# Kernel tuning notes

Measured on AMD Instinct MI355X. Metric: run time of the kernel, lower is better.

Reference implementation:

```python
import jax, jax.numpy as jnp
import numpy as np
from jax import lax

V, D, H, HR = 32000, 512, 1024, 2
T_SRC, T_TGT, T_REF, B, NREF = 128, 128, 32, 64, 4


def _gru_scan(x_emb, lengths, h0, Wih, Whh, bih, bhh):
    """Masked GRU over padded [T,B,D]; equivalent to torch pack->GRU->unpack.
    Returns (outputs [T,B,h] zeroed past lengths, final hidden [B,h])."""
    T = x_emb.shape[0]
    xW = jnp.einsum('tbd,gd->tbg', x_emb, Wih) + bih  # [T,B,3h] input-gate preacts

    def step(h, inp):
        xw, t = inp
        hw = h @ Whh.T + bhh
        xr, xz, xn = jnp.split(xw, 3, axis=-1)
        hr, hz, hn = jnp.split(hw, 3, axis=-1)
        r = jax.nn.sigmoid(xr + hr)
        z = jax.nn.sigmoid(xz + hz)
        n = jnp.tanh(xn + r * hn)
        h_new = (1.0 - z) * n + z * h
        m = (t < lengths)[:, None]
        h_next = jnp.where(m, h_new, h)   # freeze hidden past length (packing)
        out = jnp.where(m, h_new, 0.0)    # unpack pads with zeros
        return h_next, out

    hT, outs = lax.scan(step, h0, (xW, jnp.arange(T)))
    return outs, hT


def setup_inputs() -> dict:
    key = jax.random.key(0)
    ks = jax.random.split(key, 32)

    def u(k, shape, fan):
        lim = 1.0 / np.sqrt(fan)
        return jax.random.uniform(k, shape, jnp.float32, -lim, lim)

    inp = {}
    inp['tgt'] = jax.random.randint(ks[0], (T_TGT, B), 0, V)
    inp['tgt_lengths'] = jax.random.randint(ks[1], (B,), 1, T_TGT + 1)
    inp['src'] = jax.random.randint(ks[2], (T_SRC, B), 0, V)
    inp['src_lengths'] = jax.random.randint(ks[3], (B,), 1, T_SRC + 1)
    inp['ref_ids'] = jax.random.randint(ks[4], (NREF, T_REF, B), 0, V)
    inp['ref_lengths'] = jax.random.randint(ks[5], (NREF, B), 1, T_REF + 1)
    inp['emb'] = jax.random.normal(ks[6], (V, D), jnp.float32) * 0.02
    inp['src_Wih'] = u(ks[7], (3 * H, D), H)
    inp['src_Whh'] = u(ks[8], (3 * H, H), H)
    inp['src_bih'] = u(ks[9], (3 * H,), H)
    inp['src_bhh'] = u(ks[10], (3 * H,), H)
    inp['tgt_Wih'] = u(ks[11], (3 * H, D), H)
    inp['tgt_Whh'] = u(ks[12], (3 * H, H), H)
    inp['tgt_bih'] = u(ks[13], (3 * H,), H)
    inp['tgt_bhh'] = u(ks[14], (3 * H,), H)
    inp['ref_Wih'] = u(ks[15], (3 * HR, D), HR)
    inp['ref_Whh'] = u(ks[16], (3 * HR, HR), HR)
    inp['ref_bih'] = u(ks[17], (3 * HR,), HR)
    inp['ref_bhh'] = u(ks[18], (3 * HR,), HR)
    inp['p1_W'] = u(ks[19], (64, H), H)
    inp['p1_b'] = u(ks[20], (64,), H)
    inp['p2_W'] = u(ks[21], (2, 64), 64)
    inp['p2_b'] = u(ks[22], (2,), 64)
    return inp


def reference(tgt, tgt_lengths, src, src_lengths, ref_ids, ref_lengths, emb,
              src_Wih, src_Whh, src_bih, src_bhh,
              tgt_Wih, tgt_Whh, tgt_bih, tgt_bhh,
              ref_Wih, ref_Whh, ref_bih, ref_bhh,
              p1_W, p1_b, p2_W, p2_b):
    # --- src encoder ---
    src_emb = emb[src]  # [T_SRC,B,D]
    h0 = jnp.zeros((src.shape[1], src_Whh.shape[1]), emb.dtype)
    _, src_hT = _gru_scan(src_emb, src_lengths, h0, src_Wih, src_Whh, src_bih, src_bhh)

    # --- ref encoders: original loops in Python over the ref list with
    # per-ref sort/pack/tiny-GRU; here vectorized with vmap over NREF.
    # (Output is computed, as torch eager does, but does not feed logits.)
    ref_emb = emb[ref_ids]  # [NREF,T_REF,B,D]
    h0r = jnp.zeros((ref_ids.shape[2], ref_Whh.shape[1]), emb.dtype)
    ref_context, ref_hidden = jax.vmap(
        lambda e, l: _gru_scan(e, l, h0r, ref_Wih, ref_Whh, ref_bih, ref_bhh)
    )(ref_emb, ref_lengths)
    del ref_context, ref_hidden

    # --- tgt decoder initialized from src final hidden ---
    tgt_emb = emb[tgt]
    _, tgt_hT = _gru_scan(tgt_emb, tgt_lengths, src_hT, tgt_Wih, tgt_Whh, tgt_bih, tgt_bhh)

    # --- projection head (dropout = identity in eval) ---
    logits = jnp.tanh(tgt_hT @ p1_W.T + p1_b) @ p2_W.T + p2_b  # [B,2]
    return logits
```

## Files before the change

kernel.cpp:

```cpp
#include <hip/hip_runtime.h>
#include <stdint.h>

typedef short short8 __attribute__((ext_vector_type(8)));
typedef float f32x4 __attribute__((ext_vector_type(4)));
typedef float f32x2 __attribute__((ext_vector_type(2)));
typedef unsigned long long u64;

#define TSEQ   128
#define BATCH  64
#define DIM    512
#define HID    1024
#define G3     3072
#define MROWS  (TSEQ * BATCH)
#define NB     32
#define HB     32

__device__ __forceinline__ unsigned short f2bf(float f) {
  union { float f; unsigned u; } v; v.f = f;
  unsigned u = v.u;
  return (unsigned short)((u + 0x7FFFu + ((u >> 16) & 1u)) >> 16);
}

__device__ __forceinline__ short8 pack8(f32x4 a, f32x4 b) {
  short8 r;
  r[0] = (short)f2bf(a.x); r[1] = (short)f2bf(a.y);
  r[2] = (short)f2bf(a.z); r[3] = (short)f2bf(a.w);
  r[4] = (short)f2bf(b.x); r[5] = (short)f2bf(b.y);
  r[6] = (short)f2bf(b.z); r[7] = (short)f2bf(b.w);
  return r;
}

__device__ __forceinline__ u64 packbf4(float a, float b, float c, float d) {
  return (u64)f2bf(a) | ((u64)f2bf(b) << 16) | ((u64)f2bf(c) << 32) | ((u64)f2bf(d) << 48);
}

__device__ __forceinline__ float sigm(float x) { return 1.0f / (1.0f + __expf(-x)); }
__device__ __forceinline__ float tanh_fast(float x) { return 2.0f / (1.0f + __expf(-2.0f * x)) - 1.0f; }

__global__ __launch_bounds__(256) void prep_kernel(
    const int* __restrict__ ids, const float* __restrict__ emb,
    const float* __restrict__ wih, unsigned short* __restrict__ X,
    unsigned short* __restrict__ Wb, unsigned int* bars, int nbar)
{
  int row = blockIdx.x;
  int tid = threadIdx.x;
  const float* srcp;
  unsigned short* dst;
  if (row < MROWS) {
    srcp = emb + (long)ids[row] * DIM;
    dst  = X + (long)row * DIM;
  } else {
    int wr = row - MROWS;
    srcp = wih + (long)wr * DIM;
    dst  = Wb + (long)wr * DIM;
  }
  int d = tid * 2;
  f32x2 v = *(const f32x2*)(srcp + d);
  unsigned pk = (unsigned)f2bf(v.x) | ((unsigned)f2bf(v.y) << 16);
  *(unsigned*)(dst + d) = pk;
  if (bars != nullptr && row == 0 && tid < nbar) bars[tid] = 0u;
}

#define BM 128
#define BN 128
#define BK 32

__global__ __launch_bounds__(256) void xw_gemm(
    const unsigned short* __restrict__ X,
    const unsigned short* __restrict__ W,
    const float* __restrict__ bih,
    float* __restrict__ out)
{
  __shared__ unsigned short As[BM * BK];
  __shared__ unsigned short Bs[BN * BK];
  int tid = threadIdx.x;
  int w = tid >> 6, l = tid & 63;
  int m0 = blockIdx.y * BM;
  int n0 = blockIdx.x * BN;
  int wr = w >> 1, wc = w & 1;

  int sr = tid >> 2, skq = tid & 3;
  int sr2 = sr + 64;
  int sgk  = (skq - (sr  >> 1)) & 3;
  int sgk2 = (skq - (sr2 >> 1)) & 3;
  const unsigned short* gA0 = X + (long)(m0 + sr ) * DIM + sgk  * 8;
  const unsigned short* gA1 = X + (long)(m0 + sr2) * DIM + sgk2 * 8;
  const unsigned short* gB0 = W + (long)(n0 + sr ) * DIM + sgk  * 8;
  const unsigned short* gB1 = W + (long)(n0 + sr2) * DIM + sgk2 * 8;
  unsigned short* lA0 = As + sr  * BK + skq * 8;
  unsigned short* lA1 = As + sr2 * BK + skq * 8;
  unsigned short* lB0 = Bs + sr  * BK + skq * 8;
  unsigned short* lB1 = Bs + sr2 * BK + skq * 8;

  f32x4 acc[4][4];
  #pragma unroll
  for (int mt = 0; mt < 4; ++mt)
    #pragma unroll
    for (int nt = 0; nt < 4; ++nt) acc[mt][nt] = (f32x4){};

  short8 va0 = *(const short8*)(gA0);
  short8 va1 = *(const short8*)(gA1);
  short8 vb0 = *(const short8*)(gB0);
  short8 vb1 = *(const short8*)(gB1);

  int fr = l & 15, fk = l >> 4;
  for (int kt = 0; kt < DIM / BK; ++kt) {
    __syncthreads();
    *(short8*)lA0 = va0; *(short8*)lA1 = va1;
    *(short8*)lB0 = vb0; *(short8*)lB1 = vb1;
    __syncthreads();
    if (kt + 1 < DIM / BK) {
      int ko = (kt + 1) * BK;
      va0 = *(const short8*)(gA0 + ko);
      va1 = *(const short8*)(gA1 + ko);
      vb0 = *(const short8*)(gB0 + ko);
      vb1 = *(const short8*)(gB1 + ko);
    }
    short8 af[4], bf[4];
    #pragma unroll
    for (int mt = 0; mt < 4; ++mt) {
      int r = wr * 64 + mt * 16 + fr;
      int slot = ((r >> 1) + fk) & 3;
      af[mt] = *(const short8*)(As + r * BK + slot * 8);
    }
    #pragma unroll
    for (int nt = 0; nt < 4; ++nt) {
      int r = wc * 64 + nt * 16 + fr;
      int slot = ((r >> 1) + fk) & 3;
      bf[nt] = *(const short8*)(Bs + r * BK + slot * 8);
    }
    #pragma unroll
    for (int mt = 0; mt < 4; ++mt)
      #pragma unroll
      for (int nt = 0; nt < 4; ++nt)
        acc[mt][nt] = __builtin_amdgcn_mfma_f32_16x16x32_bf16(af[mt], bf[nt], acc[mt][nt], 0, 0, 0);
  }

  #pragma unroll
  for (int nt = 0; nt < 4; ++nt) {
    int n = n0 + wc * 64 + nt * 16 + fr;
    float bias = bih[n];
    #pragma unroll
    for (int mt = 0; mt < 4; ++mt) {
      int mbase = m0 + wr * 64 + mt * 16 + fk * 4;
      #pragma unroll
      for (int r = 0; r < 4; ++r)
        out[(long)(mbase + r) * G3 + n] = acc[mt][nt][r] + bias;
    }
  }
}

#define MF(a, b, c) __builtin_amdgcn_mfma_f32_16x16x32_bf16(a, b, c, 0, 0, 0)

#define ISSUE(ss, kk) do { \
  asm volatile("global_load_dwordx4 %0, %1, off offset:%2 sc0 sc1" \
               : "=v"(bv[ss][0]) : "v"(ad0), "i"((kk) * 64) : "memory"); \
  asm volatile("global_load_dwordx4 %0, %1, off offset:%2 sc0 sc1" \
               : "=v"(bv[ss][1]) : "v"(ad1), "i"((kk) * 64) : "memory"); \
  asm volatile("global_load_dwordx4 %0, %1, off offset:%2 sc0 sc1" \
               : "=v"(bv[ss][2]) : "v"(ad2), "i"((kk) * 64) : "memory"); \
  asm volatile("global_load_dwordx4 %0, %1, off offset:%2 sc0 sc1" \
               : "=v"(bv[ss][3]) : "v"(ad3), "i"((kk) * 64) : "memory"); \
} while (0)

#define MF6(kk, ss, nt) \
  acc[0][nt] = MF(areg[0][kk], bv[ss][nt], acc[0][nt]); \
  acc[1][nt] = MF(areg[1][kk], bv[ss][nt], acc[1][nt]); \
  acc[2][nt] = MF(areg[2][kk], bv[ss][nt], acc[2][nt]); \
  acc[3][nt] = MF(areg[3][kk], bv[ss][nt], acc[3][nt]); \
  acc[4][nt] = MF(areg[4][kk], bv[ss][nt], acc[4][nt]); \
  acc[5][nt] = MF(areg[5][kk], bv[ss][nt], acc[5][nt]);

#define CONS(kk, ss, wn) do { \
  asm volatile("s_waitcnt vmcnt(" #wn ")" ::: "memory"); \
  __builtin_amdgcn_sched_barrier(0); \
  MF6(kk, ss, 0) MF6(kk, ss, 1) MF6(kk, ss, 2) MF6(kk, ss, 3) \
} while (0)

#define CONSI(kk, ss, wn, nk) do { CONS(kk, ss, wn); ISSUE(ss, nk); } while (0)

__global__ __launch_bounds__(256, 1) void gru_kernel(
    const float* __restrict__ Whh, const float* __restrict__ bhh,
    const float* __restrict__ xw, const int* __restrict__ lengths,
    u64* __restrict__ hbf,
    float* __restrict__ hf32,
    unsigned int* __restrict__ bar, int T, int initzero)
{
  const int tid = threadIdx.x;
  const int w = tid >> 6, l = tid & 63;
  const int fr = l & 15, fk = l >> 4;
  const int U0 = blockIdx.x * HB;

  short8 areg[6][8];
  #pragma unroll
  for (int mt = 0; mt < 6; ++mt) {
    const int m = mt * 16 + fr;
    const int gate = m >> 5, u = m & 31;
    const float* wp = Whh + (size_t)(gate * HID + U0 + u) * HID + w * 256 + fk * 8;
    #pragma unroll
    for (int ksl = 0; ksl < 8; ++ksl) {
      f32x4 a0 = *(const f32x4*)(wp + ksl * 32);
      f32x4 a1 = *(const f32x4*)(wp + ksl * 32 + 4);
      areg[mt][ksl] = pack8(a0, a1);
    }
  }

  const int gb = l;
  const int j0 = w * 8;
  const size_t hoff = (size_t)gb * (HID / 4) + (size_t)(U0 + j0) / 4;
  const int len_b = lengths[gb];

  float h[8];
  #pragma unroll
  for (int j = 0; j < 8; ++j)
    h[j] = initzero ? 0.0f : hf32[(size_t)gb * HID + U0 + j0 + j];

  __shared__ float red[2][96][67];
  __shared__ float bb[3][32];
  if (tid < 96) bb[tid >> 5][tid & 31] = bhh[(tid >> 5) * HID + U0 + (tid & 31)];

  f32x4 xrv[2], xzv[2], xnv[2];
  #define LOAD_XW(tt) do { \
    const float* xp_ = xw + ((size_t)(tt) * BATCH + gb) * G3 + U0 + j0; \
    xrv[0] = *(const f32x4*)(xp_);            xrv[1] = *(const f32x4*)(xp_ + 4); \
    xzv[0] = *(const f32x4*)(xp_ + HID);      xzv[1] = *(const f32x4*)(xp_ + HID + 4); \
    xnv[0] = *(const f32x4*)(xp_ + 2 * HID);  xnv[1] = *(const f32x4*)(xp_ + 2 * HID + 4); \
  } while (0)

  {
    union { u64 q[2]; f32x4 v4; } pk;
    pk.q[0] = packbf4(h[0], h[1], h[2], h[3]);
    pk.q[1] = packbf4(h[4], h[5], h[6], h[7]);
    uint64_t hw = (uint64_t)(hbf + hoff);
    asm volatile("global_store_dwordx4 %0, %1, off sc0 sc1" :: "v"(hw), "v"(pk.v4) : "memory");
    asm volatile("s_waitcnt vmcnt(0)" ::: "memory");
    __syncthreads();
    if (tid == 0)
      __hip_atomic_fetch_add(bar, 1u, __ATOMIC_RELAXED, __HIP_MEMORY_SCOPE_AGENT);
    LOAD_XW(0);
    if (tid == 0) {
      while (__hip_atomic_load(bar, __ATOMIC_RELAXED, __HIP_MEMORY_SCOPE_AGENT) < (unsigned)NB)
        __builtin_amdgcn_s_sleep(1);
    }
    __syncthreads();
  }

  for (int t = 0; t < T; ++t) {
    asm volatile("s_waitcnt vmcnt(0)" ::: "memory");

    const char* hbase = (const char*)hbf + (size_t)(t & 1) * (BATCH * (HID / 4) * 8);
    uint64_t ad0 = (uint64_t)(hbase + (size_t)(fr) * 2048 + w * 512 + fk * 16);
    uint64_t ad1 = ad0 + 16 * 2048;
    uint64_t ad2 = ad0 + 32 * 2048;
    uint64_t ad3 = ad0 + 48 * 2048;

    f32x4 acc[6][4];
    #pragma unroll
    for (int mt = 0; mt < 6; ++mt)
      #pragma unroll
      for (int nt = 0; nt < 4; ++nt) acc[mt][nt] = (f32x4){};

    short8 bv[6][4];
    ISSUE(0, 0); ISSUE(1, 1); ISSUE(2, 2); ISSUE(3, 3); ISSUE(4, 4); ISSUE(5, 5);
    CONSI(0, 0, 20, 6);
    CONSI(1, 1, 20, 7);
    CONS(2, 2, 20);
    CONS(3, 3, 16);
    CONS(4, 4, 12);
    CONS(5, 5, 8);
    CONS(6, 0, 4);
    CONS(7, 1, 0);

    if (w < 2) {
      #pragma unroll
      for (int mt = 0; mt < 6; ++mt)
        #pragma unroll
        for (int nt = 0; nt < 4; ++nt)
          #pragma unroll
          for (int r = 0; r < 4; ++r)
            red[w][mt * 16 + fk * 4 + r][nt * 16 + fr] = acc[mt][nt][r];
    }
    __syncthreads();
    if (w >= 2) {
      #pragma unroll
      for (int mt = 0; mt < 6; ++mt)
        #pragma unroll
        for (int nt = 0; nt < 4; ++nt)
          #pragma unroll
          for (int r = 0; r < 4; ++r)
            red[w - 2][mt * 16 + fk * 4 + r][nt * 16 + fr] += acc[mt][nt][r];
    }
    __syncthreads();

    const int upd = (t < len_b);
    #pragma unroll
    for (int j = 0; j < 8; ++j) {
      const int u = j0 + j;
      float hrv = red[0][u][gb]      + red[1][u][gb]      + bb[0][u];
      float hzv = red[0][32 + u][gb] + red[1][32 + u][gb] + bb[1][u];
      float hnv = red[0][64 + u][gb] + red[1][64 + u][gb] + bb[2][u];
      float rr = sigm(xrv[j >> 2][j & 3] + hrv);
      float zz = sigm(xzv[j >> 2][j & 3] + hzv);
      float nn = tanh_fast(xnv[j >> 2][j & 3] + rr * hnv);
      float cc = (1.0f - zz) * nn + zz * h[j];
      h[j] = upd ? cc : h[j];
    }

    if (t + 1 < T) {
      union { u64 q[2]; f32x4 v4; } pk;
      pk.q[0] = packbf4(h[0], h[1], h[2], h[3]);
      pk.q[1] = packbf4(h[4], h[5], h[6], h[7]);
      uint64_t hw = (uint64_t)((char*)hbf + (size_t)((t + 1) & 1) * (BATCH * (HID / 4) * 8) + hoff * 8);
      asm volatile("global_store_dwordx4 %0, %1, off sc0 sc1" :: "v"(hw), "v"(pk.v4) : "memory");
      asm volatile("s_waitcnt vmcnt(0)" ::: "memory");
      __syncthreads();
      if (tid == 0)
        __hip_atomic_fetch_add(bar, 1u, __ATOMIC_RELAXED, __HIP_MEMORY_SCOPE_AGENT);
      LOAD_XW(t + 1);
      if (tid == 0) {
        const unsigned target = (unsigned)(t + 2) * (unsigned)NB;
        while (__hip_atomic_load(bar, __ATOMIC_RELAXED, __HIP_MEMORY_SCOPE_AGENT) < target)
          __builtin_amdgcn_s_sleep(1);
      }
      __syncthreads();
    }
  }

  #pragma unroll
  for (int j = 0; j < 8; ++j)
    hf32[(size_t)gb * HID + U0 + j0 + j] = h[j];
}

__global__ __launch_bounds__(256) void head_kernel(
    const float* __restrict__ hf32, const float* __restrict__ p1W,
    const float* __restrict__ p1b, const float* __restrict__ p2W,
    const float* __restrict__ p2b, float* __restrict__ outp)
{
  int b = blockIdx.x;
  int tid = threadIdx.x;
  __shared__ float hrow[HID];
  __shared__ float red[4][64];
  __shared__ float s1[64];
  for (int d = tid; d < HID; d += 256) hrow[d] = hf32[(long)b * HID + d];
  __syncthreads();
  int j = tid & 63, q = tid >> 6;
  const float* wrow = p1W + (long)j * HID + q * 256;
  float s = 0.0f;
  for (int k = 0; k < 256; ++k) s += hrow[q * 256 + k] * wrow[k];
  red[q][j] = s;
  __syncthreads();
  if (tid < 64) {
    float v = red[0][tid] + red[1][tid] + red[2][tid] + red[3][tid] + p1b[tid];
    s1[tid] = tanh_fast(v);
  }
  __syncthreads();
  if (tid < 2) {
    float a = p2b[tid];
    for (int k = 0; k < 64; ++k) a += s1[k] * p2W[tid * 64 + k];
    outp[b * 2 + tid] = a;
  }
}

extern "C" void kernel_launch(void* const* d_in, const int* in_sizes, int n_in,
                              void* d_out, int out_size, void* d_ws, size_t ws_size,
                              hipStream_t stream) {
  const int*   tgt_ids = (const int*)d_in[0];
  const int*   tgt_len = (const int*)d_in[1];
  const int*   src_ids = (const int*)d_in[2];
  const int*   src_len = (const int*)d_in[3];
  const float* emb  = (const float*)d_in[6];
  const float* sWih = (const float*)d_in[7];
  const float* sWhh = (const float*)d_in[8];
  const float* sbih = (const float*)d_in[9];
  const float* sbhh = (const float*)d_in[10];
  const float* tWih = (const float*)d_in[11];
  const float* tWhh = (const float*)d_in[12];
  const float* tbih = (const float*)d_in[13];
  const float* tbhh = (const float*)d_in[14];
  const float* p1W  = (const float*)d_in[19];
  const float* p1b  = (const float*)d_in[20];
  const float* p2W  = (const float*)d_in[21];
  const float* p2b  = (const float*)d_in[22];

  char* ws = (char*)d_ws;
  size_t off = 0;
  float* xw = (float*)(ws + off);                   off += (size_t)MROWS * G3 * 4;
  unsigned short* X  = (unsigned short*)(ws + off); off += (size_t)MROWS * DIM * 2;
  unsigned short* Wb = (unsigned short*)(ws + off); off += (size_t)G3 * DIM * 2;
  u64* hbf = (u64*)(ws + off);                      off += 2ull * BATCH * (HID / 4) * 8;
  float* hf32 = (float*)(ws + off);                 off += (size_t)BATCH * HID * 4;
  unsigned int* bars = (unsigned int*)(ws + off);   off += 256;
  if (ws_size < off) return;

  const int PREP_BLOCKS = MROWS + G3;

  prep_kernel<<<PREP_BLOCKS, 256, 0, stream>>>(src_ids, emb, sWih, X, Wb, bars, 64);
  xw_gemm<<<dim3(G3 / BN, MROWS / BM), 256, 0, stream>>>(X, Wb, sbih, xw);
  gru_kernel<<<NB, 256, 0, stream>>>(sWhh, sbhh, xw, src_len, hbf, hf32, bars, TSEQ, 1);
  prep_kernel<<<PREP_BLOCKS, 256, 0, stream>>>(tgt_ids, emb, tWih, X, Wb, nullptr, 0);
  xw_gemm<<<dim3(G3 / BN, MROWS / BM), 256, 0, stream>>>(X, Wb, tbih, xw);
  gru_kernel<<<NB, 256, 0, stream>>>(tWhh, tbhh, xw, tgt_len, hbf, hf32, bars + 32, TSEQ, 0);
  head_kernel<<<BATCH, 256, 0, stream>>>(hf32, p1W, p1b, p2W, p2b, (float*)d_out);
}
```

Baseline: 2.518 ms.

## Replace atomic-counter grid barrier with per-block flag barrier and single-pass LDS reduction

The grid-wide step barrier in the persistent GRU kernel now has each block write its step number to its own padded flag slot. Waiting threads poll all 32 flags in parallel with wave-wide any, then invalidate the cache, instead of one thread spinning with sleeps on a shared atomic counter. The cross-wave partial-sum reduction changes from two serialized LDS phases to all four waves writing vectorized partials and summing them in one pass, which removes a __syncthreads per step. The h loads drop the sc1 bit and rely on the explicit buffer_inv after the barrier. This adds LDS use and memory-ordering risk in exchange for lower per-step latency.

Measured after the change: 2.316 ms. -8.0%, faster.

```diff
diff --git a/kernel.cpp b/kernel.cpp
--- a/kernel.cpp
+++ b/kernel.cpp
@@ -40,7 +40,7 @@
 __global__ __launch_bounds__(256) void prep_kernel(
     const int* __restrict__ ids, const float* __restrict__ emb,
     const float* __restrict__ wih, unsigned short* __restrict__ X,
-    unsigned short* __restrict__ Wb, unsigned int* bars, int nbar)
+    unsigned short* __restrict__ Wb, unsigned int* bars)
 {
   int row = blockIdx.x;
   int tid = threadIdx.x;
@@ -58,7 +58,7 @@
   f32x2 v = *(const f32x2*)(srcp + d);
   unsigned pk = (unsigned)f2bf(v.x) | ((unsigned)f2bf(v.y) << 16);
   *(unsigned*)(dst + d) = pk;
-  if (bars != nullptr && row == 0 && tid < nbar) bars[tid] = 0u;
+  if (bars != nullptr && row == 0) ((f32x4*)bars)[tid] = (f32x4){};
 }
 
 #define BM 128
@@ -153,13 +153,13 @@
 #define MF(a, b, c) __builtin_amdgcn_mfma_f32_16x16x32_bf16(a, b, c, 0, 0, 0)
 
 #define ISSUE(ss, kk) do { \
-  asm volatile("global_load_dwordx4 %0, %1, off offset:%2 sc0 sc1" \
+  asm volatile("global_load_dwordx4 %0, %1, off offset:%2 sc0" \
                : "=v"(bv[ss][0]) : "v"(ad0), "i"((kk) * 64) : "memory"); \
-  asm volatile("global_load_dwordx4 %0, %1, off offset:%2 sc0 sc1" \
+  asm volatile("global_load_dwordx4 %0, %1, off offset:%2 sc0" \
                : "=v"(bv[ss][1]) : "v"(ad1), "i"((kk) * 64) : "memory"); \
-  asm volatile("global_load_dwordx4 %0, %1, off offset:%2 sc0 sc1" \
+  asm volatile("global_load_dwordx4 %0, %1, off offset:%2 sc0" \
                : "=v"(bv[ss][2]) : "v"(ad2), "i"((kk) * 64) : "memory"); \
-  asm volatile("global_load_dwordx4 %0, %1, off offset:%2 sc0 sc1" \
+  asm volatile("global_load_dwordx4 %0, %1, off offset:%2 sc0" \
                : "=v"(bv[ss][3]) : "v"(ad3), "i"((kk) * 64) : "memory"); \
 } while (0)
 
@@ -178,6 +178,29 @@
 } while (0)
 
 #define CONSI(kk, ss, wn, nk) do { CONS(kk, ss, wn); ISSUE(ss, nk); } while (0)
+
+#define BARRIER_ARRIVE(tgtv) do { \
+  asm volatile("s_waitcnt vmcnt(0)" ::: "memory"); \
+  __syncthreads(); \
+  if (tid == 0) { \
+    unsigned fv_ = (unsigned)(tgtv); \
+    uint64_t fa_ = (uint64_t)(bar + (blockIdx.x << 4)); \
+    asm volatile("global_store_dword %0, %1, off sc0 sc1" :: "v"(fa_), "v"(fv_) : "memory"); \
+  } \
+} while (0)
+
+#define BARRIER_WAIT(tgtv) do { \
+  if (tid < NB) { \
+    unsigned v_; \
+    uint64_t pa_ = (uint64_t)(bar + (tid << 4)); \
+    do { \
+      asm volatile("global_load_dword %0, %1, off sc0 sc1" : "=v"(v_) : "v"(pa_) : "memory"); \
+      asm volatile("s_waitcnt vmcnt(0)" ::: "memory"); \
+    } while (__any(v_ < (unsigned)(tgtv))); \
+  } \
+  __syncthreads(); \
+  asm volatile("buffer_inv sc1" ::: "memory"); \
+} while (0)
 
 __global__ __launch_bounds__(256, 1) void gru_kernel(
     const float* __restrict__ Whh, const float* __restrict__ bhh,
@@ -215,7 +238,7 @@
   for (int j = 0; j < 8; ++j)
     h[j] = initzero ? 0.0f : hf32[(size_t)gb * HID + U0 + j0 + j];
 
-  __shared__ float red[2][96][67];
+  __shared__ float red2[4][64][100];
   __shared__ float bb[3][32];
   if (tid < 96) bb[tid >> 5][tid & 31] = bhh[(tid >> 5) * HID + U0 + (tid & 31)];
 
@@ -233,16 +256,9 @@
     pk.q[1] = packbf4(h[4], h[5], h[6], h[7]);
     uint64_t hw = (uint64_t)(hbf + hoff);
     asm volatile("global_store_dwordx4 %0, %1, off sc0 sc1" :: "v"(hw), "v"(pk.v4) : "memory");
-    asm volatile("s_waitcnt vmcnt(0)" ::: "memory");
-    __syncthreads();
-    if (tid == 0)
-      __hip_atomic_fetch_add(bar, 1u, __ATOMIC_RELAXED, __HIP_MEMORY_SCOPE_AGENT);
+    BARRIER_ARRIVE(1);
     LOAD_XW(0);
-    if (tid == 0) {
-      while (__hip_atomic_load(bar, __ATOMIC_RELAXED, __HIP_MEMORY_SCOPE_AGENT) < (unsigned)NB)
-        __builtin_amdgcn_s_sleep(1);
-    }
-    __syncthreads();
+    BARRIER_WAIT(1);
   }
 
   for (int t = 0; t < T; ++t) {
@@ -271,37 +287,29 @@
     CONS(6, 0, 4);
     CONS(7, 1, 0);
 
-    if (w < 2) {
+    #pragma unroll
+    for (int mt = 0; mt < 6; ++mt)
       #pragma unroll
-      for (int mt = 0; mt < 6; ++mt)
-        #pragma unroll
-        for (int nt = 0; nt < 4; ++nt)
-          #pragma unroll
-          for (int r = 0; r < 4; ++r)
-            red[w][mt * 16 + fk * 4 + r][nt * 16 + fr] = acc[mt][nt][r];
-    }
+      for (int nt = 0; nt < 4; ++nt)
+        *(f32x4*)&red2[w][nt * 16 + fr][mt * 16 + fk * 4] = acc[mt][nt];
     __syncthreads();
-    if (w >= 2) {
-      #pragma unroll
-      for (int mt = 0; mt < 6; ++mt)
-        #pragma unroll
-        for (int nt = 0; nt < 4; ++nt)
-          #pragma unroll
-          for (int r = 0; r < 4; ++r)
-            red[w - 2][mt * 16 + fk * 4 + r][nt * 16 + fr] += acc[mt][nt][r];
-    }
-    __syncthreads();
+
+    #define RD4(s, row) (*(const f32x4*)&red2[s][gb][row])
+    f32x4 sr_[2], sz_[2], sn_[2];
+    #pragma unroll
+    for (int hh = 0; hh < 2; ++hh) {
+      const int rbase = j0 + hh * 4;
+      sr_[hh] = RD4(0, rbase)      + RD4(1, rbase)      + RD4(2, rbase)      + RD4(3, rbase)      + *(const f32x4*)&bb[0][rbase];
+      sz_[hh] = RD4(0, 32 + rbase) + RD4(1, 32 + rbase) + RD4(2, 32 + rbase) + RD4(3, 32 + rbase) + *(const f32x4*)&bb[1][rbase];
+      sn_[hh] = RD4(0, 64 + rbase) + RD4(1, 64 + rbase) + RD4(2, 64 + rbase) + RD4(3, 64 + rbase) + *(const f32x4*)&bb[2][rbase];
+    }
 
     const int upd = (t < len_b);
     #pragma unroll
     for (int j = 0; j < 8; ++j) {
-      const int u = j0 + j;
-      float hrv = red[0][u][gb]      + red[1][u][gb]      + bb[0][u];
-      float hzv = red[0][32 + u][gb] + red[1][32 + u][gb] + bb[1][u];
-      float hnv = red[0][64 + u][gb] + red[1][64 + u][gb] + bb[2][u];
-      float rr = sigm(xrv[j >> 2][j & 3] + hrv);
-      float zz = sigm(xzv[j >> 2][j & 3] + hzv);
-      float nn = tanh_fast(xnv[j >> 2][j & 3] + rr * hnv);
+      float rr = sigm(xrv[j >> 2][j & 3] + sr_[j >> 2][j & 3]);
+      float zz = sigm(xzv[j >> 2][j & 3] + sz_[j >> 2][j & 3]);
+      float nn = tanh_fast(xnv[j >> 2][j & 3] + rr * sn_[j >> 2][j & 3]);
       float cc = (1.0f - zz) * nn + zz * h[j];
       h[j] = upd ? cc : h[j];
     }
@@ -312,17 +320,9 @@
       pk.q[1] = packbf4(h[4], h[5], h[6], h[7]);
       uint64_t hw = (uint64_t)((char*)hbf + (size_t)((t + 1) & 1) * (BATCH * (HID / 4) * 8) + hoff * 8);
       asm volatile("global_store_dwordx4 %0, %1, off sc0 sc1" :: "v"(hw), "v"(pk.v4) : "memory");
-      asm volatile("s_waitcnt vmcnt(0)" ::: "memory");
-      __syncthreads();
-      if (tid == 0)
-        __hip_atomic_fetch_add(bar, 1u, __ATOMIC_RELAXED, __HIP_MEMORY_SCOPE_AGENT);
+      BARRIER_ARRIVE(t + 2);
       LOAD_XW(t + 1);
-      if (tid == 0) {
-        const unsigned target = (unsigned)(t + 2) * (unsigned)NB;
-        while (__hip_atomic_load(bar, __ATOMIC_RELAXED, __HIP_MEMORY_SCOPE_AGENT) < target)
-          __builtin_amdgcn_s_sleep(1);
-      }
-      __syncthreads();
+      BARRIER_WAIT(t + 2);
     }
   }
 
@@ -389,16 +389,16 @@
   unsigned short* Wb = (unsigned short*)(ws + off); off += (size_t)G3 * DIM * 2;
   u64* hbf = (u64*)(ws + off);                      off += 2ull * BATCH * (HID / 4) * 8;
   float* hf32 = (float*)(ws + off);                 off += (size_t)BATCH * HID * 4;
-  unsigned int* bars = (unsigned int*)(ws + off);   off += 256;
+  unsigned int* bars = (unsigned int*)(ws + off);   off += 4096;
   if (ws_size < off) return;
 
   const int PREP_BLOCKS = MROWS + G3;
 
-  prep_kernel<<<PREP_BLOCKS, 256, 0, stream>>>(src_ids, emb, sWih, X, Wb, bars, 64);
+  prep_kernel<<<PREP_BLOCKS, 256, 0, stream>>>(src_ids, emb, sWih, X, Wb, bars);
   xw_gemm<<<dim3(G3 / BN, MROWS / BM), 256, 0, stream>>>(X, Wb, sbih, xw);
   gru_kernel<<<NB, 256, 0, stream>>>(sWhh, sbhh, xw, src_len, hbf, hf32, bars, TSEQ, 1);
-  prep_kernel<<<PREP_BLOCKS, 256, 0, stream>>>(tgt_ids, emb, tWih, X, Wb, nullptr, 0);
+  prep_kernel<<<PREP_BLOCKS, 256, 0, stream>>>(tgt_ids, emb, tWih, X, Wb, nullptr);
   xw_gemm<<<dim3(G3 / BN, MROWS / BM), 256, 0, stream>>>(X, Wb, tbih, xw);
-  gru_kernel<<<NB, 256, 0, stream>>>(tWhh, tbhh, xw, tgt_len, hbf, hf32, bars + 32, TSEQ, 0);
+  gru_kernel<<<NB, 256, 0, stream>>>(tWhh, tbhh, xw, tgt_len, hbf, hf32, bars + 512, TSEQ, 0);
   head_kernel<<<BATCH, 256, 0, stream>>>(hf32, p1W, p1b, p2W, p2b, (float*)d_out);
 }
```

## Split GRU batch into two halves pipelined across separate flag barriers

Applied to the files above, without the earlier changes.

The persistent GRU kernel now processes the batch as two 32-column halves, each with its own per-block flag barrier (generation stores to padded slots instead of a shared atomic counter). While one half's hidden state is being published and waited on, the other half's matmul runs, so barrier latency is meant to overlap with compute. The cross-warp reduction changes from a two-stage add to a four-way vectorized LDS sum. In exchange there are more barriers and syncthreads per step, a larger flags buffer that must be zeroed, and polling by 32 lanes per block.

Result: faster. 2.400 ms (-4.7%).

```diff
diff --git a/kernel.cpp b/kernel.cpp
--- a/kernel.cpp
+++ b/kernel.cpp
@@ -40,7 +40,7 @@
 __global__ __launch_bounds__(256) void prep_kernel(
     const int* __restrict__ ids, const float* __restrict__ emb,
     const float* __restrict__ wih, unsigned short* __restrict__ X,
-    unsigned short* __restrict__ Wb, unsigned int* bars, int nbar)
+    unsigned short* __restrict__ Wb, unsigned int* bars)
 {
   int row = blockIdx.x;
   int tid = threadIdx.x;
@@ -58,7 +58,10 @@
   f32x2 v = *(const f32x2*)(srcp + d);
   unsigned pk = (unsigned)f2bf(v.x) | ((unsigned)f2bf(v.y) << 16);
   *(unsigned*)(dst + d) = pk;
-  if (bars != nullptr && row == 0 && tid < nbar) bars[tid] = 0u;
+  if (bars != nullptr && row == 0) {
+    #pragma unroll
+    for (int k = 0; k < 4; ++k) ((f32x4*)bars)[k * 256 + tid] = (f32x4){};
+  }
 }
 
 #define BM 128
@@ -152,32 +155,55 @@
 
 #define MF(a, b, c) __builtin_amdgcn_mfma_f32_16x16x32_bf16(a, b, c, 0, 0, 0)
 
-#define ISSUE(ss, kk) do { \
+#define ISSUE2(ss, kk) do { \
   asm volatile("global_load_dwordx4 %0, %1, off offset:%2 sc0 sc1" \
                : "=v"(bv[ss][0]) : "v"(ad0), "i"((kk) * 64) : "memory"); \
   asm volatile("global_load_dwordx4 %0, %1, off offset:%2 sc0 sc1" \
                : "=v"(bv[ss][1]) : "v"(ad1), "i"((kk) * 64) : "memory"); \
-  asm volatile("global_load_dwordx4 %0, %1, off offset:%2 sc0 sc1" \
-               : "=v"(bv[ss][2]) : "v"(ad2), "i"((kk) * 64) : "memory"); \
-  asm volatile("global_load_dwordx4 %0, %1, off offset:%2 sc0 sc1" \
-               : "=v"(bv[ss][3]) : "v"(ad3), "i"((kk) * 64) : "memory"); \
 } while (0)
 
-#define MF6(kk, ss, nt) \
-  acc[0][nt] = MF(areg[0][kk], bv[ss][nt], acc[0][nt]); \
-  acc[1][nt] = MF(areg[1][kk], bv[ss][nt], acc[1][nt]); \
-  acc[2][nt] = MF(areg[2][kk], bv[ss][nt], acc[2][nt]); \
-  acc[3][nt] = MF(areg[3][kk], bv[ss][nt], acc[3][nt]); \
-  acc[4][nt] = MF(areg[4][kk], bv[ss][nt], acc[4][nt]); \
-  acc[5][nt] = MF(areg[5][kk], bv[ss][nt], acc[5][nt]);
-
-#define CONS(kk, ss, wn) do { \
+#define MF12(kk, ss) \
+  acc[0][0] = MF(areg[0][kk], bv[ss][0], acc[0][0]); \
+  acc[1][0] = MF(areg[1][kk], bv[ss][0], acc[1][0]); \
+  acc[2][0] = MF(areg[2][kk], bv[ss][0], acc[2][0]); \
+  acc[3][0] = MF(areg[3][kk], bv[ss][0], acc[3][0]); \
+  acc[4][0] = MF(areg[4][kk], bv[ss][0], acc[4][0]); \
+  acc[5][0] = MF(areg[5][kk], bv[ss][0], acc[5][0]); \
+  acc[0][1] = MF(areg[0][kk], bv[ss][1], acc[0][1]); \
+  acc[1][1] = MF(areg[1][kk], bv[ss][1], acc[1][1]); \
+  acc[2][1] = MF(areg[2][kk], bv[ss][1], acc[2][1]); \
+  acc[3][1] = MF(areg[3][kk], bv[ss][1], acc[3][1]); \
+  acc[4][1] = MF(areg[4][kk], bv[ss][1], acc[4][1]); \
+  acc[5][1] = MF(areg[5][kk], bv[ss][1], acc[5][1]);
+
+#define CONS2(kk, ss, wn) do { \
   asm volatile("s_waitcnt vmcnt(" #wn ")" ::: "memory"); \
   __builtin_amdgcn_sched_barrier(0); \
-  MF6(kk, ss, 0) MF6(kk, ss, 1) MF6(kk, ss, 2) MF6(kk, ss, 3) \
+  MF12(kk, ss) \
 } while (0)
 
-#define CONSI(kk, ss, wn, nk) do { CONS(kk, ss, wn); ISSUE(ss, nk); } while (0)
+#define CONSI2(kk, ss, wn, nk) do { CONS2(kk, ss, wn); ISSUE2(ss, nk); } while (0)
+
+__device__ __forceinline__ void bar_arrive(unsigned* flags, int rank, unsigned gen, int tid) {
+  asm volatile("s_waitcnt vmcnt(0)" ::: "memory");
+  __syncthreads();
+  if (tid == 0) {
+    uint64_t fa = (uint64_t)(flags + (rank << 4));
+    asm volatile("global_store_dword %0, %1, off sc0 sc1" :: "v"(fa), "v"(gen) : "memory");
+  }
+}
+
+__device__ __forceinline__ void bar_wait(unsigned* flags, unsigned gen, int tid) {
+  if (tid < NB) {
+    unsigned v;
+    uint64_t pa = (uint64_t)(flags + (tid << 4));
+    do {
+      asm volatile("global_load_dword %0, %1, off sc0 sc1" : "=v"(v) : "v"(pa) : "memory");
+      asm volatile("s_waitcnt vmcnt(0)" ::: "memory");
+    } while (__any(v < gen));
+  }
+  __syncthreads();
+}
 
 __global__ __launch_bounds__(256, 1) void gru_kernel(
     const float* __restrict__ Whh, const float* __restrict__ bhh,
@@ -190,6 +216,10 @@
   const int w = tid >> 6, l = tid & 63;
   const int fr = l & 15, fk = l >> 4;
   const int U0 = blockIdx.x * HB;
+  const int rank = blockIdx.x;
+
+  unsigned* barA = bar;
+  unsigned* barB = bar + 1024;
 
   short8 areg[6][8];
   #pragma unroll
@@ -205,130 +235,149 @@
     }
   }
 
-  const int gb = l;
-  const int j0 = w * 8;
-  const size_t hoff = (size_t)gb * (HID / 4) + (size_t)(U0 + j0) / 4;
-  const int len_b = lengths[gb];
-
-  float h[8];
+  const int gb2 = tid & 31;
+  const int j0u = (tid >> 5) * 4;
+  const int bA = gb2, bB = 32 + gb2;
+  const size_t hoffA = (size_t)bA * (HID / 4) + (size_t)(U0 + j0u) / 4;
+  const size_t hoffB = (size_t)bB * (HID / 4) + (size_t)(U0 + j0u) / 4;
+  const int lenA = lengths[bA], lenB = lengths[bB];
+
+  float hA[4], hB[4];
   #pragma unroll
-  for (int j = 0; j < 8; ++j)
-    h[j] = initzero ? 0.0f : hf32[(size_t)gb * HID + U0 + j0 + j];
-
-  __shared__ float red[2][96][67];
+  for (int j = 0; j < 4; ++j) {
+    hA[j] = initzero ? 0.0f : hf32[(size_t)bA * HID + U0 + j0u + j];
+    hB[j] = initzero ? 0.0f : hf32[(size_t)bB * HID + U0 + j0u + j];
+  }
+
+  __shared__ float red2[4][32][100];
   __shared__ float bb[3][32];
   if (tid < 96) bb[tid >> 5][tid & 31] = bhh[(tid >> 5) * HID + U0 + (tid & 31)];
-
-  f32x4 xrv[2], xzv[2], xnv[2];
-  #define LOAD_XW(tt) do { \
-    const float* xp_ = xw + ((size_t)(tt) * BATCH + gb) * G3 + U0 + j0; \
-    xrv[0] = *(const f32x4*)(xp_);            xrv[1] = *(const f32x4*)(xp_ + 4); \
-    xzv[0] = *(const f32x4*)(xp_ + HID);      xzv[1] = *(const f32x4*)(xp_ + HID + 4); \
-    xnv[0] = *(const f32x4*)(xp_ + 2 * HID);  xnv[1] = *(const f32x4*)(xp_ + 2 * HID + 4); \
+  __syncthreads();
+
+  const f32x4 bbr = *(const f32x4*)&bb[0][j0u];
+  const f32x4 bbz = *(const f32x4*)&bb[1][j0u];
+  const f32x4 bbn = *(const f32x4*)&bb[2][j0u];
+
+  f32x4 xrA, xzA, xnA, xrB, xzB, xnB;
+  #define LOAD_XWA(tt) do { \
+    const float* xp_ = xw + ((size_t)(tt) * BATCH + bA) * G3 + U0 + j0u; \
+    xrA = *(const f32x4*)(xp_); xzA = *(const f32x4*)(xp_ + HID); xnA = *(const f32x4*)(xp_ + 2 * HID); \
   } while (0)
+  #define LOAD_XWB(tt) do { \
+    const float* xp_ = xw + ((size_t)(tt) * BATCH + bB) * G3 + U0 + j0u; \
+    xrB = *(const f32x4*)(xp_); xzB = *(const f32x4*)(xp_ + HID); xnB = *(const f32x4*)(xp_ + 2 * HID); \
+  } while (0)
 
   {
-    union { u64 q[2]; f32x4 v4; } pk;
-    pk.q[0] = packbf4(h[0], h[1], h[2], h[3]);
-    pk.q[1] = packbf4(h[4], h[5], h[6], h[7]);
-    uint64_t hw = (uint64_t)(hbf + hoff);
-    asm volatile("global_store_dwordx4 %0, %1, off sc0 sc1" :: "v"(hw), "v"(pk.v4) : "memory");
-    asm volatile("s_waitcnt vmcnt(0)" ::: "memory");
-    __syncthreads();
-    if (tid == 0)
-      __hip_atomic_fetch_add(bar, 1u, __ATOMIC_RELAXED, __HIP_MEMORY_SCOPE_AGENT);
-    LOAD_XW(0);
+    u64 pA = packbf4(hA[0], hA[1], hA[2], hA[3]);
+    u64 pB = packbf4(hB[0], hB[1], hB[2], hB[3]);
+    uint64_t aA = (uint64_t)(hbf + hoffA), aB = (uint64_t)(hbf + hoffB);
+    asm volatile("global_store_dwordx2 %0, %1, off sc0 sc1" :: "v"(aA), "v"(pA) : "memory");
+    asm volatile("global_store_dwordx2 %0, %1, off sc0 sc1" :: "v"(aB), "v"(pB) : "memory");
+    bar_arrive(barA, rank, 1u, tid);
     if (tid == 0) {
-      while (__hip_atomic_load(bar, __ATOMIC_RELAXED, __HIP_MEMORY_SCOPE_AGENT) < (unsigned)NB)
-        __builtin_amdgcn_s_sleep(1);
-    }
-    __syncthreads();
+      uint64_t fb = (uint64_t)(barB + (rank << 4));
+      unsigned g1 = 1u;
+      asm volatile("global_store_dword %0, %1, off sc0 sc1" :: "v"(fb), "v"(g1) : "memory");
+    }
+    LOAD_XWA(0); LOAD_XWB(0);
+    bar_wait(barA, 1u, tid);
   }
 
   for (int t = 0; t < T; ++t) {
-    asm volatile("s_waitcnt vmcnt(0)" ::: "memory");
-
     const char* hbase = (const char*)hbf + (size_t)(t & 1) * (BATCH * (HID / 4) * 8);
-    uint64_t ad0 = (uint64_t)(hbase + (size_t)(fr) * 2048 + w * 512 + fk * 16);
-    uint64_t ad1 = ad0 + 16 * 2048;
-    uint64_t ad2 = ad0 + 32 * 2048;
-    uint64_t ad3 = ad0 + 48 * 2048;
-
-    f32x4 acc[6][4];
-    #pragma unroll
-    for (int mt = 0; mt < 6; ++mt)
-      #pragma unroll
-      for (int nt = 0; nt < 4; ++nt) acc[mt][nt] = (f32x4){};
-
-    short8 bv[6][4];
-    ISSUE(0, 0); ISSUE(1, 1); ISSUE(2, 2); ISSUE(3, 3); ISSUE(4, 4); ISSUE(5, 5);
-    CONSI(0, 0, 20, 6);
-    CONSI(1, 1, 20, 7);
-    CONS(2, 2, 20);
-    CONS(3, 3, 16);
-    CONS(4, 4, 12);
-    CONS(5, 5, 8);
-    CONS(6, 0, 4);
-    CONS(7, 1, 0);
-
-    if (w < 2) {
-      #pragma unroll
-      for (int mt = 0; mt < 6; ++mt)
-        #pragma unroll
-        for (int nt = 0; nt < 4; ++nt)
-          #pragma unroll
-          for (int r = 0; r < 4; ++r)
-            red[w][mt * 16 + fk * 4 + r][nt * 16 + fr] = acc[mt][nt][r];
-    }
-    __syncthreads();
-    if (w >= 2) {
-      #pragma unroll
-      for (int mt = 0; mt < 6; ++mt)
-        #pragma unroll
-        for (int nt = 0; nt < 4; ++nt)
-          #pragma unroll
-          for (int r = 0; r < 4; ++r)
-            red[w - 2][mt * 16 + fk * 4 + r][nt * 16 + fr] += acc[mt][nt][r];
-    }
-    __syncthreads();
-
-    const int upd = (t < len_b);
-    #pragma unroll
-    for (int j = 0; j < 8; ++j) {
-      const int u = j0 + j;
-      float hrv = red[0][u][gb]      + red[1][u][gb]      + bb[0][u];
-      float hzv = red[0][32 + u][gb] + red[1][32 + u][gb] + bb[1][u];
-      float hnv = red[0][64 + u][gb] + red[1][64 + u][gb] + bb[2][u];
-      float rr = sigm(xrv[j >> 2][j & 3] + hrv);
-      float zz = sigm(xzv[j >> 2][j & 3] + hzv);
-      float nn = tanh_fast(xnv[j >> 2][j & 3] + rr * hnv);
-      float cc = (1.0f - zz) * nn + zz * h[j];
-      h[j] = upd ? cc : h[j];
-    }
-
-    if (t + 1 < T) {
-      union { u64 q[2]; f32x4 v4; } pk;
-      pk.q[0] = packbf4(h[0], h[1], h[2], h[3]);
-      pk.q[1] = packbf4(h[4], h[5], h[6], h[7]);
-      uint64_t hw = (uint64_t)((char*)hbf + (size_t)((t + 1) & 1) * (BATCH * (HID / 4) * 8) + hoff * 8);
-      asm volatile("global_store_dwordx4 %0, %1, off sc0 sc1" :: "v"(hw), "v"(pk.v4) : "memory");
+    char* hnext = (char*)hbf + (size_t)((t + 1) & 1) * (BATCH * (HID / 4) * 8);
+    const int tail = (t + 1 < T);
+
+    {
       asm volatile("s_waitcnt vmcnt(0)" ::: "memory");
-      __syncthreads();
-      if (tid == 0)
-        __hip_atomic_fetch_add(bar, 1u, __ATOMIC_RELAXED, __HIP_MEMORY_SCOPE_AGENT);
-      LOAD_XW(t + 1);
-      if (tid == 0) {
-        const unsigned target = (unsigned)(t + 2) * (unsigned)NB;
-        while (__hip_atomic_load(bar, __ATOMIC_RELAXED, __HIP_MEMORY_SCOPE_AGENT) < target)
-          __builtin_amdgcn_s_sleep(1);
+      uint64_t ad0 = (uint64_t)(hbase + (size_t)fr * 2048 + w * 512 + fk * 16);
+      uint64_t ad1 = ad0 + 16 * 2048;
+      f32x4 acc[6][2];
+      #pragma unroll
+      for (int mt = 0; mt < 6; ++mt) { acc[mt][0] = (f32x4){}; acc[mt][1] = (f32x4){}; }
+      short8 bv[6][2];
+      ISSUE2(0, 0); ISSUE2(1, 1); ISSUE2(2, 2); ISSUE2(3, 3); ISSUE2(4, 4); ISSUE2(5, 5);
+      CONSI2(0, 0, 10, 6); CONSI2(1, 1, 10, 7);
+      CONS2(2, 2, 10); CONS2(3, 3, 8); CONS2(4, 4, 6); CONS2(5, 5, 4); CONS2(6, 0, 2); CONS2(7, 1, 0);
+
+      #pragma unroll
+      for (int mt = 0; mt < 6; ++mt) {
+        *(f32x4*)&red2[w][fr][mt * 16 + fk * 4]      = acc[mt][0];
+        *(f32x4*)&red2[w][16 + fr][mt * 16 + fk * 4] = acc[mt][1];
       }
       __syncthreads();
+      #define RD4(s, row) (*(const f32x4*)&red2[s][gb2][row])
+      f32x4 sr_ = RD4(0, j0u)      + RD4(1, j0u)      + RD4(2, j0u)      + RD4(3, j0u)      + bbr;
+      f32x4 sz_ = RD4(0, 32 + j0u) + RD4(1, 32 + j0u) + RD4(2, 32 + j0u) + RD4(3, 32 + j0u) + bbz;
+      f32x4 sn_ = RD4(0, 64 + j0u) + RD4(1, 64 + j0u) + RD4(2, 64 + j0u) + RD4(3, 64 + j0u) + bbn;
+      const int upd = (t < lenA);
+      #pragma unroll
+      for (int j = 0; j < 4; ++j) {
+        float rr = sigm(xrA[j] + sr_[j]);
+        float zz = sigm(xzA[j] + sz_[j]);
+        float nn = tanh_fast(xnA[j] + rr * sn_[j]);
+        float cc = (1.0f - zz) * nn + zz * hA[j];
+        hA[j] = upd ? cc : hA[j];
+      }
+      __syncthreads();
+    }
+    if (tail) {
+      u64 pA = packbf4(hA[0], hA[1], hA[2], hA[3]);
+      uint64_t aA = (uint64_t)(hnext + hoffA * 8);
+      asm volatile("global_store_dwordx2 %0, %1, off sc0 sc1" :: "v"(aA), "v"(pA) : "memory");
+      bar_arrive(barA, rank, (unsigned)(t + 2), tid);
+      LOAD_XWA(t + 1);
+    }
+    bar_wait(barB, (unsigned)(t + 1), tid);
+
+    {
+      asm volatile("s_waitcnt vmcnt(0)" ::: "memory");
+      uint64_t ad0 = (uint64_t)(hbase + (size_t)(32 + fr) * 2048 + w * 512 + fk * 16);
+      uint64_t ad1 = ad0 + 16 * 2048;
+      f32x4 acc[6][2];
+      #pragma unroll
+      for (int mt = 0; mt < 6; ++mt) { acc[mt][0] = (f32x4){}; acc[mt][1] = (f32x4){}; }
+      short8 bv[6][2];
+      ISSUE2(0, 0); ISSUE2(1, 1); ISSUE2(2, 2); ISSUE2(3, 3); ISSUE2(4, 4); ISSUE2(5, 5);
+      CONSI2(0, 0, 10, 6); CONSI2(1, 1, 10, 7);
+      CONS2(2, 2, 10); CONS2(3, 3, 8); CONS2(4, 4, 6); CONS2(5, 5, 4); CONS2(6, 0, 2); CONS2(7, 1, 0);
+
+      #pragma unroll
+      for (int mt = 0; mt < 6; ++mt) {
+        *(f32x4*)&red2[w][fr][mt * 16 + fk * 4]      = acc[mt][0];
+        *(f32x4*)&red2[w][16 + fr][mt * 16 + fk * 4] = acc[mt][1];
+      }
+      __syncthreads();
+      f32x4 sr_ = RD4(0, j0u)      + RD4(1, j0u)      + RD4(2, j0u)      + RD4(3, j0u)      + bbr;
+      f32x4 sz_ = RD4(0, 32 + j0u) + RD4(1, 32 + j0u) + RD4(2, 32 + j0u) + RD4(3, 32 + j0u) + bbz;
+      f32x4 sn_ = RD4(0, 64 + j0u) + RD4(1, 64 + j0u) + RD4(2, 64 + j0u) + RD4(3, 64 + j0u) + bbn;
+      const int upd = (t < lenB);
+      #pragma unroll
+      for (int j = 0; j < 4; ++j) {
+        float rr = sigm(xrB[j] + sr_[j]);
+        float zz = sigm(xzB[j] + sz_[j]);
+        float nn = tanh_fast(xnB[j] + rr * sn_[j]);
+        float cc = (1.0f - zz) * nn + zz * hB[j];
+        hB[j] = upd ? cc : hB[j];
+      }
+      __syncthreads();
+    }
+    if (tail) {
+      u64 pB = packbf4(hB[0], hB[1], hB[2], hB[3]);
+      uint64_t aB = (uint64_t)(hnext + hoffB * 8);
+      asm volatile("global_store_dwordx2 %0, %1, off sc0 sc1" :: "v"(aB), "v"(pB) : "memory");
+      bar_arrive(barB, rank, (unsigned)(t + 2), tid);
+      LOAD_XWB(t + 1);
+      bar_wait(barA, (unsigned)(t + 2), tid);
     }
   }
 
   #pragma unroll
-  for (int j = 0; j < 8; ++j)
-    hf32[(size_t)gb * HID + U0 + j0 + j] = h[j];
+  for (int j = 0; j < 4; ++j) {
+    hf32[(size_t)bA * HID + U0 + j0u + j] = hA[j];
+    hf32[(size_t)bB * HID + U0 + j0u + j] = hB[j];
+  }
 }
 
 __global__ __launch_bounds__(256) void head_kernel(
@@ -389,16 +438,16 @@
   unsigned short* Wb = (unsigned short*)(ws + off); off += (size_t)G3 * DIM * 2;
   u64* hbf = (u64*)(ws + off);                      off += 2ull * BATCH * (HID / 4) * 8;
   float* hf32 = (float*)(ws + off);                 off += (size_t)BATCH * HID * 4;
-  unsigned int* bars = (unsigned int*)(ws + off);   off += 256;
+  unsigned int* bars = (unsigned int*)(ws + off);   off += 16384;
   if (ws_size < off) return;
 
   const int PREP_BLOCKS = MROWS + G3;
 
-  prep_kernel<<<PREP_BLOCKS, 256, 0, stream>>>(src_ids, emb, sWih, X, Wb, bars, 64);
+  prep_kernel<<<PREP_BLOCKS, 256, 0, stream>>>(src_ids, emb, sWih, X, Wb, bars);
   xw_gemm<<<dim3(G3 / BN, MROWS / BM), 256, 0, stream>>>(X, Wb, sbih, xw);
   gru_kernel<<<NB, 256, 0, stream>>>(sWhh, sbhh, xw, src_len, hbf, hf32, bars, TSEQ, 1);
-  prep_kernel<<<PREP_BLOCKS, 256, 0, stream>>>(tgt_ids, emb, tWih, X, Wb, nullptr, 0);
+  prep_kernel<<<PREP_BLOCKS, 256, 0, stream>>>(tgt_ids, emb, tWih, X, Wb, nullptr);
   xw_gemm<<<dim3(G3 / BN, MROWS / BM), 256, 0, stream>>>(X, Wb, tbih, xw);
-  gru_kernel<<<NB, 256, 0, stream>>>(tWhh, tbhh, xw, tgt_len, hbf, hf32, bars + 32, TSEQ, 0);
+  gru_kernel<<<NB, 256, 0, stream>>>(tWhh, tbhh, xw, tgt_len, hbf, hf32, bars + 2048, TSEQ, 0);
   head_kernel<<<BATCH, 256, 0, stream>>>(hf32, p1W, p1b, p2W, p2b, (float*)d_out);
 }
```
